# Optimization experiments

Hardware: AMD Instinct MI355X
Metric: run time of the kernel (lower is better)

## Reference

```python
import jax, jax.numpy as jnp
import numpy as np

B, S, HID = 2, 2048, 2048
H, KV, D = 16, 8, 128
EPS = 1e-6
MROPE = [21, 21, 22]  # half_dim=64 -> [64//3, 64//3, 64-2*(64//3)]
SCALE = D ** -0.5


def setup_inputs() -> dict:
    key = jax.random.key(0)
    ks = jax.random.split(key, 8)
    hidden_states = jax.random.normal(ks[0], (B, S, HID), jnp.float32)
    # 3D mrope cos/sin: one position grid per modality axis (use same arange positions)
    inv_freq = 1.0 / (10000.0 ** (jnp.arange(0, D, 2, dtype=jnp.float32) / D))  # [64]
    pos = jnp.arange(S, dtype=jnp.float32)
    freqs = pos[:, None] * inv_freq[None, :]                  # [S, 64]
    emb = jnp.concatenate([freqs, freqs], axis=-1)            # [S, 128]
    cos = jnp.broadcast_to(jnp.cos(emb)[None, None], (3, B, S, D)).astype(jnp.float32)
    sin = jnp.broadcast_to(jnp.sin(emb)[None, None], (3, B, S, D)).astype(jnp.float32)
    q_w = jax.random.normal(ks[1], (H * D, HID), jnp.float32) * 0.02
    k_w = jax.random.normal(ks[2], (KV * D, HID), jnp.float32) * 0.02
    v_w = jax.random.normal(ks[3], (KV * D, HID), jnp.float32) * 0.02
    o_w = jax.random.normal(ks[4], (HID, H * D), jnp.float32) * 0.02
    q_norm_w = jnp.ones((D,), jnp.float32)
    k_norm_w = jnp.ones((D,), jnp.float32)
    return dict(hidden_states=hidden_states, cos=cos, sin=sin, q_w=q_w, k_w=k_w,
                v_w=v_w, o_w=o_w, q_norm_w=q_norm_w, k_norm_w=k_norm_w)


def _rmsnorm(x, w):
    var = jnp.mean(jnp.square(x.astype(jnp.float32)), axis=-1, keepdims=True)
    return (x * jax.lax.rsqrt(var + EPS)).astype(x.dtype) * w


def _rotate_half(x):
    x1, x2 = jnp.split(x, 2, axis=-1)
    return jnp.concatenate([-x2, x1], axis=-1)


def _mrope_mix(t):
    # t: [3, B, S, D]; split last dim into mrope_section*2 chunks, pick chunk i from axis-0 index i%3
    sections = MROPE * 2
    idx = np.cumsum(sections)[:-1]
    chunks = jnp.split(t, idx, axis=-1)
    mixed = jnp.concatenate([c[i % 3] for i, c in enumerate(chunks)], axis=-1)  # [B, S, D]
    return mixed[:, None, :, :]  # unsqueeze head dim -> [B, 1, S, D]


def reference(hidden_states, cos, sin, q_w, k_w, v_w, o_w, q_norm_w, k_norm_w):
    # QKV projections -> [B, n_heads, S, D]
    q = (hidden_states @ q_w.T).reshape(B, S, H, D)
    k = (hidden_states @ k_w.T).reshape(B, S, KV, D)
    v = (hidden_states @ v_w.T).reshape(B, S, KV, D)
    q = _rmsnorm(q, q_norm_w).transpose(0, 2, 1, 3)   # [B, H, S, D]
    k = _rmsnorm(k, k_norm_w).transpose(0, 2, 1, 3)   # [B, KV, S, D]
    v = v.transpose(0, 2, 1, 3)                       # [B, KV, S, D]
    # 3D multimodal RoPE
    c = _mrope_mix(cos)
    s = _mrope_mix(sin)
    q = q * c + _rotate_half(q) * s
    k = k * c + _rotate_half(k) * s
    # GQA: repeat kv heads
    groups = H // KV
    k = jnp.repeat(k, groups, axis=1)  # [B, H, S, D]
    v = jnp.repeat(v, groups, axis=1)
    # causal SDPA (eager)
    scores = jnp.einsum('bhqd,bhkd->bhqk', q, k) * SCALE
    causal = jnp.tril(jnp.ones((S, S), bool))
    scores = jnp.where(causal[None, None], scores, jnp.finfo(scores.dtype).min)
    probs = jax.nn.softmax(scores, axis=-1)
    attn = jnp.einsum('bhqk,bhkd->bhqd', probs, v)     # [B, H, S, D]
    attn = attn.transpose(0, 2, 1, 3).reshape(B, S, H * D)
    return attn @ o_w.T
```

## Files before the change

kernel.cpp:

```cpp
#include <hip/hip_runtime.h>
#include <hip/hip_bf16.h>

typedef __attribute__((ext_vector_type(8))) short short8;
typedef __attribute__((ext_vector_type(4))) short short4v;
typedef __attribute__((ext_vector_type(4))) float f32x4;

#define B_ 2
#define S_ 2048
#define HID_ 2048
#define H_ 16
#define KV_ 8
#define D_ 128
#define SCALE_ 0.08838834764831845f

__device__ inline short f2bf(float f) {
    union { __hip_bfloat16 h; short s; } u;
    u.h = __float2bfloat16(f);
    return u.s;
}
__device__ inline float bf2f(short s) {
    union { short s; __hip_bfloat16 h; } u;
    u.s = s;
    return __bfloat162float(u.h);
}

__device__ inline void gld16(const short* g, short* l) {
    __builtin_amdgcn_global_load_lds(
        (const __attribute__((address_space(1))) unsigned int*)g,
        (__attribute__((address_space(3))) unsigned int*)l, 16, 0, 0);
}

__device__ inline int mrope_axis(int d) {
    int m = d & 63;
    return m < 21 ? 0 : (m < 42 ? 1 : 2);
}
__global__ __launch_bounds__(256) void prep(const float* __restrict__ hid,
                                            const float* __restrict__ qw_,
                                            const float* __restrict__ kw_,
                                            const float* __restrict__ vw_,
                                            const float* __restrict__ ow_,
                                            const float* __restrict__ cosp,
                                            const float* __restrict__ sinp,
                                            short* __restrict__ Hb,
                                            short* __restrict__ Wqkv,
                                            short* __restrict__ Owb,
                                            float* __restrict__ cm,
                                            float* __restrict__ sm) {
    int bid = blockIdx.x;
    if (bid < 20480) {
        const float* src; short* dst; int base;
        if (bid < 8192)       { src = hid; dst = Hb;              base = bid; }
        else if (bid < 12288) { src = qw_; dst = Wqkv;            base = bid - 8192; }
        else if (bid < 14336) { src = kw_; dst = Wqkv + 4194304;  base = bid - 12288; }
        else if (bid < 16384) { src = vw_; dst = Wqkv + 6291456;  base = bid - 14336; }
        else                  { src = ow_; dst = Owb;             base = bid - 16384; }
        int i = base * 1024 + threadIdx.x * 4;
        float4 v = *(const float4*)(&src[i]);
        short4v o;
        o.x = f2bf(v.x); o.y = f2bf(v.y); o.z = f2bf(v.z); o.w = f2bf(v.w);
        *(short4v*)(&dst[i]) = o;
    } else {
        const size_t AX = (size_t)B_ * S_ * D_;
        int i0 = (bid - 20480) * 1024 + threadIdx.x * 4;
#pragma unroll
        for (int k = 0; k < 4; ++k) {
            int idx = i0 + k;
            int d = idx & (D_ - 1);
            size_t src = (size_t)mrope_axis(d) * AX + idx;
            cm[idx] = cosp[src];
            sm[idx] = sinp[src];
        }
    }
}

__global__ __launch_bounds__(256) void gemm_bt(const short* __restrict__ A,
                                               const short* __restrict__ B,
                                               float* __restrict__ C,
                                               int M, int N, int K) {
    __shared__ __align__(16) short As[128 * 64];
    __shared__ __align__(16) short Bs[128 * 64];
    int tid = threadIdx.x;
    int wave = tid >> 6, lane = tid & 63;
    int m16 = lane & 15, quad = lane >> 4;
    int wr = wave >> 1, wc = wave & 1;
    int m0 = blockIdx.y * 128, n0 = blockIdx.x * 128;
    int srow = lane >> 3;
    int scol = ((lane & 7) ^ srow) << 3;
    f32x4 acc[4][4] = {};
    for (int k0 = 0; k0 < K; k0 += 64) {
#pragma unroll
        for (int i = 0; i < 4; ++i) {
            gld16(&A[(size_t)(m0 + wave * 32 + i * 8 + srow) * K + k0 + scol],
                  &As[(wave * 32 + i * 8) * 64]);
            gld16(&B[(size_t)(n0 + wave * 32 + i * 8 + srow) * K + k0 + scol],
                  &Bs[(wave * 32 + i * 8) * 64]);
        }
        __syncthreads();
        short8 a[4][2], b[4][2];
#pragma unroll
        for (int i = 0; i < 4; ++i)
#pragma unroll
            for (int kk = 0; kk < 2; ++kk) {
                int gsw = (((kk << 2) + quad) ^ (m16 & 7)) << 3;
                a[i][kk] = *(const short8*)(&As[(wr * 64 + i * 16 + m16) * 64 + gsw]);
                b[i][kk] = *(const short8*)(&Bs[(wc * 64 + i * 16 + m16) * 64 + gsw]);
            }
#pragma unroll
        for (int kk = 0; kk < 2; ++kk)
#pragma unroll
            for (int i = 0; i < 4; ++i)
#pragma unroll
                for (int j = 0; j < 4; ++j)
                    acc[i][j] = __builtin_amdgcn_mfma_f32_16x16x32_bf16(a[i][kk], b[j][kk],
                                                                        acc[i][j], 0, 0, 0);
        __syncthreads();
    }
#pragma unroll
    for (int i = 0; i < 4; ++i) {
        int row = m0 + wr * 64 + i * 16 + quad * 4;
#pragma unroll
        for (int j = 0; j < 4; ++j) {
            int col = n0 + wc * 64 + j * 16 + m16;
#pragma unroll
            for (int r = 0; r < 4; ++r)
                C[(size_t)(row + r) * N + col] = acc[i][j][r];
        }
    }
}


#define VM4 asm volatile("s_waitcnt vmcnt(4)" ::: "memory")
#define VM2 asm volatile("s_waitcnt vmcnt(2)" ::: "memory")
#define VM0 asm volatile("s_waitcnt vmcnt(0)" ::: "memory")

#define LDA(dst, QI)                                                               \
    _Pragma("unroll") for (int ii = 0; ii < 4; ++ii)                               \
        _Pragma("unroll") for (int kk = 0; kk < 2; ++kk)                           \
            dst[ii][kk] = *(const short8*)&lds[RA +                                \
                (wr * 128 + ((QI) * 4 + ii) * 16 + m16) * 64 +                     \
                ((((kk << 2) + quad) ^ (m16 & 7)) << 3)]

#define LDB(dst, QJ)                                                               \
    _Pragma("unroll") for (int jj = 0; jj < 2; ++jj)                               \
        _Pragma("unroll") for (int kk = 0; kk < 2; ++kk)                           \
            dst[jj][kk] = *(const short8*)&lds[RB +                                \
                ((QJ) * 128 + wc * 32 + jj * 16 + m16) * 64 +                      \
                ((((kk << 2) + quad) ^ (m16 & 7)) << 3)]

#define MM(ua, ub, QI, QJ)                                                         \
    _Pragma("unroll") for (int kk = 0; kk < 2; ++kk)                               \
        _Pragma("unroll") for (int ii = 0; ii < 4; ++ii)                           \
            _Pragma("unroll") for (int jj = 0; jj < 2; ++jj)                       \
                acc[(QI) * 4 + ii][(QJ) * 2 + jj] =                                \
                    __builtin_amdgcn_mfma_f32_16x16x32_bf16(                       \
                        ua[ii][kk], ub[jj][kk],                                    \
                        acc[(QI) * 4 + ii][(QJ) * 2 + jj], 0, 0, 0)

#define STGA(q) do {                                                               \
    int r_ = (wave << 3) + (lane >> 3);                                            \
    int g_ = (lane & 7) ^ (r_ & 7);                                                \
    gld16(&Am[(size_t)(m0 + (q) * 64 + r_) * 2048 + kc + (g_ << 3)],               \
          &lds[PA + (q) * 4096 + (wave << 9)]);                                    \
} while (0)
#define STGB(h, c) do {                                                            \
    int s_ = (wave << 3) + (lane >> 3);                                            \
    int sl_ = (h) * 128 + (c) * 64 + s_;                                           \
    int rr_ = ((sl_ >> 5) & 3) * 64 + (h) * 32 + (sl_ & 31);                       \
    int g_ = (lane & 7) ^ (sl_ & 7);                                               \
    gld16(&Bm[(size_t)(n0 + rr_) * 2048 + kc + (g_ << 3)],                         \
          &lds[PB + ((h) * 128 + (c) * 64) * 64 + (wave << 9)]);                   \
} while (0)

#define PH(LOADS, STG, MFMAS, WAITOP) do {                                         \
    LOADS;                                                                         \
    STG;                                                                           \
    __builtin_amdgcn_sched_barrier(0);                                             \
    __builtin_amdgcn_s_barrier();                                                  \
    asm volatile("s_waitcnt lgkmcnt(0)" ::: "memory");                             \
    __builtin_amdgcn_sched_barrier(0);                                             \
    __builtin_amdgcn_s_setprio(1);                                                 \
    MFMAS;                                                                         \
    __builtin_amdgcn_s_setprio(0);                                                 \
    WAITOP;                                                                        \
    __builtin_amdgcn_sched_barrier(0);                                             \
    __builtin_amdgcn_s_barrier();                                                  \
} while (0)

__global__ __launch_bounds__(512) void gemm_qkv(const short* __restrict__ Am,
                                                const short* __restrict__ Bm,
                                                short* __restrict__ Cq,
                                                short* __restrict__ Vb) {
    __shared__ __align__(16) char smem[131072];
    short* lds = (short*)smem;
    int tid = threadIdx.x;
    int wave = tid >> 6, lane = tid & 63;
    int m16 = lane & 15, quad = lane >> 4;
    int wr = wave >> 2, wc = wave & 3;
    int orig = blockIdx.y * 16 + blockIdx.x;
    int swz = (orig & 7) * 32 + (orig >> 3);
    int bx = swz & 15, by = swz >> 4;
    int m0 = by * 256, n0 = bx * 256;
    int x = bx;
    f32x4 acc[8][4] = {};

    {
        const int kc = 0, PA = 0, PB = 16384;
        STGA(0); STGA(1); STGA(2); STGA(3);
        STGB(0, 0); STGB(0, 1); STGB(1, 0); STGB(1, 1);
        VM0;
        __builtin_amdgcn_sched_barrier(0);
        __builtin_amdgcn_s_barrier();
    }

    short8 af[4][2], bfX[2][2], bfY[2][2];
    for (int t = 0; t < 31; ++t) {
        const int RA = (t & 1) << 15, RB = RA + 16384;
        const int PA = RA ^ 32768, PB = PA + 16384;
        const int kc = (t + 1) << 6;
        PH({ LDA(af, 0); LDB(bfX, 0); }, { STGA(0); STGA(2); },       MM(af, bfX, 0, 0), VM4);
        PH({ LDB(bfY, 1); },             { STGB(0, 0); STGB(0, 1); }, MM(af, bfY, 0, 1), VM4);
        PH({ LDA(af, 1); },              { STGB(1, 0); STGB(1, 1); }, MM(af, bfY, 1, 1), VM4);
        PH({ ; },                        { STGA(1); STGA(3); },       MM(af, bfX, 1, 0), VM4);
    }
    {
        const int RA = 32768, RB = RA + 16384;
        PH({ LDA(af, 0); LDB(bfX, 0); }, { ; }, MM(af, bfX, 0, 0), VM2);
        PH({ LDB(bfY, 1); },             { ; }, MM(af, bfY, 0, 1), VM0);
        PH({ LDA(af, 1); },              { ; }, MM(af, bfY, 1, 1), );
        PH({ ; },                        { ; }, MM(af, bfX, 1, 0), );
    }

    int bb = m0 >> 11, s0 = m0 & (S_ - 1);
    if (x >= 12) {
        short* T = (short*)smem;
        int kv0 = (x - 12) << 1;
        for (int hs = 0; hs < 2; ++hs) {
            __syncthreads();
            if (wr == hs) {
#pragma unroll
                for (int i = 0; i < 8; ++i)
#pragma unroll
                    for (int j = 0; j < 4; ++j) {
                        short4v v4;
#pragma unroll
                        for (int r = 0; r < 4; ++r) v4[r] = f2bf(acc[i][j][r]);
                        *(short4v*)&T[(wc * 64 + j * 16 + m16) * 136 + i * 16 + quad * 4] = v4;
                    }
            }
            __syncthreads();
#pragma unroll
            for (int it = 0; it < 8; ++it) {
                int e = (it * 512 + tid) * 8;
                int col = e >> 7, ro = e & 127;
                int kvh = col >> 7, d = col & 127;
                *(short8*)&Vb[(((size_t)(bb * KV_ + kv0 + kvh)) * D_ + d) * S_ +
                              s0 + hs * 128 + ro] =
                    *(const short8*)&T[col * 136 + ro];
            }
        }
    } else {
#pragma unroll
        for (int i = 0; i < 8; ++i) {
            int row = m0 + wr * 128 + i * 16 + quad * 4;
#pragma unroll
            for (int j = 0; j < 4; ++j) {
                int col = n0 + wc * 64 + j * 16 + m16;
#pragma unroll
                for (int r = 0; r < 4; ++r)
                    Cq[(size_t)(row + r) * 3072 + col] = f2bf(acc[i][j][r]);
            }
        }
    }
}

#undef PH
#undef LDA
#undef LDB
#undef MM
#undef STGA
#undef STGB
#undef VM4
#undef VM2
#undef VM0

#define TP 136
__global__ __launch_bounds__(256) void qkv_post(const short* __restrict__ Cq,
                                                const float* __restrict__ qnw,
                                                const float* __restrict__ knw,
                                                const float* __restrict__ cm,
                                                const float* __restrict__ sm,
                                                short* __restrict__ Qb,
                                                short* __restrict__ Kb) {
    __shared__ __align__(16) short T[128 * TP];
    __shared__ float sq[128];
    __shared__ float rsA[128];
    int tid = threadIdx.x;
    int hk = blockIdx.x;
    int m0 = blockIdx.y * 128;
    int b = m0 >> 11, s0 = m0 & (S_ - 1);
#pragma unroll
    for (int it = 0; it < 8; ++it) {
        int idx = it * 256 + tid;
        int row = idx >> 4, g = idx & 15;
        short8 v = *(const short8*)&Cq[(size_t)(m0 + row) * 3072 + hk * 128 + g * 8];
        *(short8*)&T[row * TP + g * 8] = v;
        float s = 0.f;
#pragma unroll
        for (int k = 0; k < 8; ++k) { float f = bf2f(v[k]); s += f * f; }
#pragma unroll
        for (int msk = 8; msk >= 1; msk >>= 1) s += __shfl_xor(s, msk, 64);
        if ((tid & 15) == 0) sq[row] = s;
    }
    __syncthreads();
    if (tid < 128) rsA[tid] = rsqrtf(sq[tid] * (1.0f / 128.0f) + 1e-6f);
    __syncthreads();
    const float* nw = (hk < 16) ? qnw : knw;
    short* outp = (hk < 16) ? (Qb + ((size_t)(b * H_ + hk)) * S_ * D_)
                            : (Kb + ((size_t)(b * KV_ + hk - 16)) * S_ * D_);
    size_t cmb = ((size_t)(b * S_ + s0)) * D_;
#pragma unroll
    for (int it = 0; it < 8; ++it) {
        int e = (it * 256 + tid) * 8;
        int row = e >> 7, colc = e & 127;
        int pc = colc ^ 64;
        float rs = rsA[row];
        float sg = (colc < 64) ? -1.f : 1.f;
        short8 nv = *(const short8*)&T[row * TP + colc];
        short8 pv = *(const short8*)&T[row * TP + pc];
        float4 cA = *(const float4*)&cm[cmb + (size_t)row * D_ + colc];
        float4 cB = *(const float4*)&cm[cmb + (size_t)row * D_ + colc + 4];
        float4 sA = *(const float4*)&sm[cmb + (size_t)row * D_ + colc];
        float4 sB = *(const float4*)&sm[cmb + (size_t)row * D_ + colc + 4];
        float4 wA = *(const float4*)&nw[colc];
        float4 wB = *(const float4*)&nw[colc + 4];
        float4 wpA = *(const float4*)&nw[pc];
        float4 wpB = *(const float4*)&nw[pc + 4];
        float cs[8] = {cA.x, cA.y, cA.z, cA.w, cB.x, cB.y, cB.z, cB.w};
        float sn[8] = {sA.x, sA.y, sA.z, sA.w, sB.x, sB.y, sB.z, sB.w};
        float wv[8] = {wA.x, wA.y, wA.z, wA.w, wB.x, wB.y, wB.z, wB.w};
        float wp[8] = {wpA.x, wpA.y, wpA.z, wpA.w, wpB.x, wpB.y, wpB.z, wpB.w};
        short8 o;
#pragma unroll
        for (int k = 0; k < 8; ++k) {
            float xv = bf2f(nv[k]) * rs * wv[k];
            float pvv = bf2f(pv[k]) * rs * wp[k];
            o[k] = f2bf(xv * cs[k] + sg * pvv * sn[k]);
        }
        *(short8*)&outp[(size_t)(s0 + row) * D_ + colc] = o;
    }
}

#define VPAD 72
__global__ __launch_bounds__(256) void attn_fa(const short* __restrict__ Qb,
                                               const short* __restrict__ Kb,
                                               const short* __restrict__ Vb,
                                               short* __restrict__ Ab) {
    __shared__ __align__(16) short Ks[2][64 * 128];
    __shared__ __align__(16) short Vs[2][128 * 64];
    __shared__ __align__(16) short Ps[4][16 * VPAD];
    int tid = threadIdx.x;
    int wave = tid >> 6, lane = tid & 63;
    int m16 = lane & 15, quad = lane >> 4;
    int bh = blockIdx.x;
    int h = bh & 15, b = bh >> 4;
    int qt = 31 - blockIdx.y;
    int kv = h >> 1;
    const short* Qp = Qb + (size_t)(b * H_ + h) * S_ * D_;
    const short* Kp = Kb + (size_t)(b * KV_ + kv) * S_ * D_;
    const short* Vp = Vb + (size_t)(b * KV_ + kv) * D_ * S_;
    int q_base = qt * 64 + wave * 16;
    int qrow = q_base + m16;
    short8 qf[4];
#pragma unroll
    for (int c = 0; c < 4; ++c)
        qf[c] = *(const short8*)(&Qp[(size_t)(q_base + m16) * D_ + c * 32 + quad * 8]);
    f32x4 o_acc[8] = {};
    float m_r = -1e30f, l_r = 0.f;
    int nchunks = qt + 1;

#pragma unroll
    for (int j = 0; j < 4; ++j) {
        int idx = wave * 4 + j;
        int r = idx * 4 + (lane >> 4);
        int g = (lane & 15) ^ (r & 7);
        gld16(&Kp[(size_t)r * D_ + g * 8], &Ks[0][idx * 512]);
    }
#pragma unroll
    for (int j = 0; j < 4; ++j) {
        int idx = wave * 4 + j;
        int r = idx * 8 + (lane >> 3);
        int g = (lane & 7) ^ (r & 7);
        gld16(&Vp[(size_t)r * S_ + g * 8], &Vs[0][idx * 512]);
    }
    __syncthreads();

    for (int kc = 0; kc < nchunks; ++kc) {
        int k0 = kc * 64;
        int cur = kc & 1;
        if (kc + 1 < nchunks) {
            int nk0 = k0 + 64, nb = cur ^ 1;
#pragma unroll
            for (int j = 0; j < 4; ++j) {
                int idx = wave * 4 + j;
                int r = idx * 4 + (lane >> 4);
                int g = (lane & 15) ^ (r & 7);
                gld16(&Kp[(size_t)(nk0 + r) * D_ + g * 8], &Ks[nb][idx * 512]);
            }
#pragma unroll
            for (int j = 0; j < 4; ++j) {
                int idx = wave * 4 + j;
                int r = idx * 8 + (lane >> 3);
                int g = (lane & 7) ^ (r & 7);
                gld16(&Vp[(size_t)r * S_ + nk0 + g * 8], &Vs[nb][idx * 512]);
            }
        }
        float sv[4][4];
        __builtin_amdgcn_s_setprio(1);
#pragma unroll
        for (int nt = 0; nt < 4; ++nt) {
            f32x4 facc = {};
#pragma unroll
            for (int c = 0; c < 4; ++c) {
                short8 kfr = *(const short8*)(&Ks[cur][(nt * 16 + m16) * 128 +
                                                      ((((c << 2) + quad) ^ (m16 & 7)) << 3)]);
                facc = __builtin_amdgcn_mfma_f32_16x16x32_bf16(kfr, qf[c], facc, 0, 0, 0);
            }
            if (kc == qt) {
#pragma unroll
                for (int r = 0; r < 4; ++r) {
                    int key = k0 + nt * 16 + quad * 4 + r;
                    sv[nt][r] = (key <= qrow) ? facc[r] * SCALE_ : -1e30f;
                }
            } else {
#pragma unroll
                for (int r = 0; r < 4; ++r) sv[nt][r] = facc[r] * SCALE_;
            }
        }
        __builtin_amdgcn_s_setprio(0);
        float mx = -1e30f;
#pragma unroll
        for (int nt = 0; nt < 4; ++nt)
#pragma unroll
            for (int r = 0; r < 4; ++r) mx = fmaxf(mx, sv[nt][r]);
        mx = fmaxf(mx, __shfl_xor(mx, 16, 64));
        mx = fmaxf(mx, __shfl_xor(mx, 32, 64));
        float m_new = fmaxf(m_r, mx);
        float alpha = __expf(m_r - m_new);
        float p[4][4], sum = 0.f;
#pragma unroll
        for (int nt = 0; nt < 4; ++nt)
#pragma unroll
            for (int r = 0; r < 4; ++r) { p[nt][r] = __expf(sv[nt][r] - m_new); sum += p[nt][r]; }
        sum += __shfl_xor(sum, 16, 64);
        sum += __shfl_xor(sum, 32, 64);
        l_r = l_r * alpha + sum;
        m_r = m_new;
#pragma unroll
        for (int nt = 0; nt < 4; ++nt) {
            short4v pk;
#pragma unroll
            for (int r = 0; r < 4; ++r) pk[r] = f2bf(p[nt][r]);
            *(short4v*)&Ps[wave][m16 * VPAD + nt * 16 + quad * 4] = pk;
        }
#pragma unroll
        for (int j = 0; j < 8; ++j) {
            f32x4 t = o_acc[j];
#pragma unroll
            for (int r = 0; r < 4; ++r) t[r] *= alpha;
            o_acc[j] = t;
        }
        __builtin_amdgcn_s_setprio(1);
#pragma unroll
        for (int kk = 0; kk < 2; ++kk) {
            short8 pf = *(const short8*)(&Ps[wave][m16 * VPAD + kk * 32 + quad * 8]);
#pragma unroll
            for (int j = 0; j < 8; ++j) {
                short8 vfr = *(const short8*)(&Vs[cur][(j * 16 + m16) * 64 +
                                                       ((((kk << 2) + quad) ^ (m16 & 7)) << 3)]);
                o_acc[j] = __builtin_amdgcn_mfma_f32_16x16x32_bf16(vfr, pf, o_acc[j], 0, 0, 0);
            }
        }
        __builtin_amdgcn_s_setprio(0);
        __syncthreads();
    }
    float inv_l = 1.0f / l_r;
    size_t base = ((size_t)(b * S_ + qrow)) * (H_ * D_) + h * D_;
#pragma unroll
    for (int j = 0; j < 8; ++j) {
        short4v ov;
#pragma unroll
        for (int r = 0; r < 4; ++r) ov[r] = f2bf(o_acc[j][r] * inv_l);
        *(short4v*)&Ab[base + j * 16 + quad * 4] = ov;
    }
}

extern "C" void kernel_launch(void* const* d_in, const int* in_sizes, int n_in,
                              void* d_out, int out_size, void* d_ws, size_t ws_size,
                              hipStream_t stream) {
    const float* hid  = (const float*)d_in[0];
    const float* cosp = (const float*)d_in[1];
    const float* sinp = (const float*)d_in[2];
    const float* q_w  = (const float*)d_in[3];
    const float* k_w  = (const float*)d_in[4];
    const float* v_w  = (const float*)d_in[5];
    const float* o_w  = (const float*)d_in[6];
    const float* qnw  = (const float*)d_in[7];
    const float* knw  = (const float*)d_in[8];

    char* w = (char*)d_ws;
    short* Hb    = (short*)w;  w += (size_t)4096 * 2048 * 2;
    short* Wqkv  = (short*)w;  w += (size_t)4096 * 2048 * 2;
    short* Owb   = (short*)w;  w += (size_t)2048 * 2048 * 2;
    short* Qb    = (short*)w;  w += (size_t)B_ * H_ * S_ * D_ * 2;
    short* Kb    = (short*)w;  w += (size_t)B_ * KV_ * S_ * D_ * 2;
    short* Vb    = (short*)w;  w += (size_t)B_ * KV_ * D_ * S_ * 2;
    short* Ab    = (short*)w;  w += (size_t)4096 * 2048 * 2;
    float* cos_m = (float*)w;  w += (size_t)B_ * S_ * D_ * 4;
    float* sin_m = (float*)w;  w += (size_t)B_ * S_ * D_ * 4;
    short* Cq    = (short*)w;  w += (size_t)4096 * 3072 * 2;

    prep<<<20992, 256, 0, stream>>>(hid, q_w, k_w, v_w, o_w, cosp, sinp,
                                    Hb, Wqkv, Owb, cos_m, sin_m);

    gemm_qkv<<<dim3(16, 16), 512, 0, stream>>>(Hb, Wqkv, Cq, Vb);

    qkv_post<<<dim3(24, 32), 256, 0, stream>>>(Cq, qnw, knw, cos_m, sin_m, Qb, Kb);

    attn_fa<<<dim3(32, 32), 256, 0, stream>>>(Qb, Kb, Vb, Ab);

    gemm_bt<<<dim3(16, 32), 256, 0, stream>>>(Ab, Owb, (float*)d_out, 4096, 2048, 2048);
}
```

Baseline: 329.6 us.

## Process two 64-row query tiles per attention block to reuse K/V tiles

Each attention block now handles 128 query rows (two 16-row subtiles per wave) so every K/V tile loaded into LDS feeds twice the MFMA work, halving the grid. Softmax switches to exp2 with a folded scale via raw v_exp_f32, and the rescale of the accumulator is skipped unless the running max grows past a threshold (lazy rescaling). The cost is doubled accumulator registers, which may lower occupancy, plus fewer blocks for load balance.

```diff
diff --git a/kernel.cpp b/kernel.cpp
--- a/kernel.cpp
+++ b/kernel.cpp
@@ -12,6 +12,8 @@
 #define KV_ 8
 #define D_ 128
 #define SCALE_ 0.08838834764831845f
+#define SC2_ 0.12751743f
+#define THRRAW_ 62.7f
 
 __device__ inline short f2bf(float f) {
     union { __hip_bfloat16 h; short s; } u;
@@ -22,6 +24,9 @@
     union { short s; __hip_bfloat16 h; } u;
     u.s = s;
     return __bfloat162float(u.h);
+}
+__device__ inline float ex2(float x) {
+    float r; asm("v_exp_f32 %0, %1" : "=v"(r) : "v"(x)); return r;
 }
 
 __device__ inline void gld16(const short* g, short* l) {
@@ -363,20 +368,22 @@
     int m16 = lane & 15, quad = lane >> 4;
     int bh = blockIdx.x;
     int h = bh & 15, b = bh >> 4;
-    int qt = 31 - blockIdx.y;
+    int qt = 15 - blockIdx.y;
     int kv = h >> 1;
     const short* Qp = Qb + (size_t)(b * H_ + h) * S_ * D_;
     const short* Kp = Kb + (size_t)(b * KV_ + kv) * S_ * D_;
     const short* Vp = Vb + (size_t)(b * KV_ + kv) * D_ * S_;
-    int q_base = qt * 64 + wave * 16;
-    int qrow = q_base + m16;
-    short8 qf[4];
-#pragma unroll
-    for (int c = 0; c < 4; ++c)
-        qf[c] = *(const short8*)(&Qp[(size_t)(q_base + m16) * D_ + c * 32 + quad * 8]);
-    f32x4 o_acc[8] = {};
-    float m_r = -1e30f, l_r = 0.f;
-    int nchunks = qt + 1;
+    int qrow0 = qt * 128 + wave * 16 + m16;
+    int qrow1 = qrow0 + 64;
+    short8 qf0[4], qf1[4];
+#pragma unroll
+    for (int c = 0; c < 4; ++c) {
+        qf0[c] = *(const short8*)(&Qp[(size_t)qrow0 * D_ + c * 32 + quad * 8]);
+        qf1[c] = *(const short8*)(&Qp[(size_t)qrow1 * D_ + c * 32 + quad * 8]);
+    }
+    f32x4 o0[8] = {}, o1[8] = {};
+    float m0r = -1e30f, l0r = 0.f, m1r = -1e30f, l1r = 0.f;
+    int nchunks = 2 * qt + 2;
 
 #pragma unroll
     for (int j = 0; j < 4; ++j) {
@@ -394,6 +401,52 @@
     }
     __syncthreads();
 
+#define SMAX(sv, mr, lr, oA, p) do {                                              \
+    float mx = -1e30f;                                                            \
+    _Pragma("unroll") for (int nt = 0; nt < 4; ++nt)                              \
+        _Pragma("unroll") for (int r = 0; r < 4; ++r) mx = fmaxf(mx, sv[nt][r]);  \
+    mx = fmaxf(mx, __shfl_xor(mx, 16, 64));                                       \
+    mx = fmaxf(mx, __shfl_xor(mx, 32, 64));                                       \
+    if (!__all(mx - mr <= THRRAW_)) {                                             \
+        float mn = fmaxf(mr, mx);                                                 \
+        float al = ex2((mr - mn) * SC2_);                                         \
+        _Pragma("unroll") for (int j = 0; j < 8; ++j) {                           \
+            f32x4 t = oA[j];                                                      \
+            _Pragma("unroll") for (int r = 0; r < 4; ++r) t[r] *= al;             \
+            oA[j] = t;                                                            \
+        }                                                                         \
+        lr *= al; mr = mn;                                                        \
+    }                                                                             \
+    float ms = mr * SC2_;                                                         \
+    float sum = 0.f;                                                              \
+    _Pragma("unroll") for (int nt = 0; nt < 4; ++nt)                              \
+        _Pragma("unroll") for (int r = 0; r < 4; ++r) {                           \
+            p[nt][r] = ex2(__builtin_fmaf(sv[nt][r], SC2_, -ms));                 \
+            sum += p[nt][r];                                                      \
+        }                                                                         \
+    sum += __shfl_xor(sum, 16, 64);                                               \
+    sum += __shfl_xor(sum, 32, 64);                                               \
+    lr += sum;                                                                    \
+} while (0)
+
+#define PVSTEP(p, oA) do {                                                        \
+    _Pragma("unroll") for (int nt = 0; nt < 4; ++nt) {                            \
+        short4v pk;                                                               \
+        _Pragma("unroll") for (int r = 0; r < 4; ++r) pk[r] = f2bf(p[nt][r]);     \
+        *(short4v*)&Ps[wave][m16 * VPAD + nt * 16 + quad * 4] = pk;               \
+    }                                                                             \
+    __builtin_amdgcn_s_setprio(1);                                                \
+    _Pragma("unroll") for (int kk = 0; kk < 2; ++kk) {                            \
+        short8 pf = *(const short8*)(&Ps[wave][m16 * VPAD + kk * 32 + quad * 8]); \
+        _Pragma("unroll") for (int j = 0; j < 8; ++j) {                           \
+            short8 vfr = *(const short8*)(&Vs[cur][(j * 16 + m16) * 64 +          \
+                                 ((((kk << 2) + quad) ^ (m16 & 7)) << 3)]);       \
+            oA[j] = __builtin_amdgcn_mfma_f32_16x16x32_bf16(vfr, pf, oA[j], 0, 0, 0); \
+        }                                                                         \
+    }                                                                             \
+    __builtin_amdgcn_s_setprio(0);                                                \
+} while (0)
+
     for (int kc = 0; kc < nchunks; ++kc) {
         int k0 = kc * 64;
         int cur = kc & 1;
@@ -414,83 +467,79 @@
                 gld16(&Vp[(size_t)r * S_ + nk0 + g * 8], &Vs[nb][idx * 512]);
             }
         }
-        float sv[4][4];
+        bool do0 = (kc < nchunks - 1);
+        bool dg0 = (kc == nchunks - 2);
+        bool dg1 = (kc == nchunks - 1);
+        float sv0[4][4], sv1[4][4];
         __builtin_amdgcn_s_setprio(1);
 #pragma unroll
         for (int nt = 0; nt < 4; ++nt) {
-            f32x4 facc = {};
-#pragma unroll
-            for (int c = 0; c < 4; ++c) {
-                short8 kfr = *(const short8*)(&Ks[cur][(nt * 16 + m16) * 128 +
-                                                      ((((c << 2) + quad) ^ (m16 & 7)) << 3)]);
-                facc = __builtin_amdgcn_mfma_f32_16x16x32_bf16(kfr, qf[c], facc, 0, 0, 0);
-            }
-            if (kc == qt) {
+            short8 kfr[4];
+#pragma unroll
+            for (int c = 0; c < 4; ++c)
+                kfr[c] = *(const short8*)(&Ks[cur][(nt * 16 + m16) * 128 +
+                                      ((((c << 2) + quad) ^ (m16 & 7)) << 3)]);
+            f32x4 f1a = {};
+#pragma unroll
+            for (int c = 0; c < 4; ++c)
+                f1a = __builtin_amdgcn_mfma_f32_16x16x32_bf16(kfr[c], qf1[c], f1a, 0, 0, 0);
+            if (do0) {
+                f32x4 f0a = {};
+#pragma unroll
+                for (int c = 0; c < 4; ++c)
+                    f0a = __builtin_amdgcn_mfma_f32_16x16x32_bf16(kfr[c], qf0[c], f0a, 0, 0, 0);
+#pragma unroll
+                for (int r = 0; r < 4; ++r) sv0[nt][r] = f0a[r];
+            }
+#pragma unroll
+            for (int r = 0; r < 4; ++r) sv1[nt][r] = f1a[r];
+        }
+        __builtin_amdgcn_s_setprio(0);
+        if (dg0) {
+#pragma unroll
+            for (int nt = 0; nt < 4; ++nt)
 #pragma unroll
                 for (int r = 0; r < 4; ++r) {
                     int key = k0 + nt * 16 + quad * 4 + r;
-                    sv[nt][r] = (key <= qrow) ? facc[r] * SCALE_ : -1e30f;
+                    if (key > qrow0) sv0[nt][r] = -1e30f;
                 }
-            } else {
-#pragma unroll
-                for (int r = 0; r < 4; ++r) sv[nt][r] = facc[r] * SCALE_;
-            }
-        }
-        __builtin_amdgcn_s_setprio(0);
-        float mx = -1e30f;
-#pragma unroll
-        for (int nt = 0; nt < 4; ++nt)
-#pragma unroll
-            for (int r = 0; r < 4; ++r) mx = fmaxf(mx, sv[nt][r]);
-        mx = fmaxf(mx, __shfl_xor(mx, 16, 64));
-        mx = fmaxf(mx, __shfl_xor(mx, 32, 64));
-        float m_new = fmaxf(m_r, mx);
-        float alpha = __expf(m_r - m_new);
-        float p[4][4], sum = 0.f;
-#pragma unroll
-        for (int nt = 0; nt < 4; ++nt)
-#pragma unroll
-            for (int r = 0; r < 4; ++r) { p[nt][r] = __expf(sv[nt][r] - m_new); sum += p[nt][r]; }
-        sum += __shfl_xor(sum, 16, 64);
-        sum += __shfl_xor(sum, 32, 64);
-        l_r = l_r * alpha + sum;
-        m_r = m_new;
-#pragma unroll
-        for (int nt = 0; nt < 4; ++nt) {
-            short4v pk;
-#pragma unroll
-            for (int r = 0; r < 4; ++r) pk[r] = f2bf(p[nt][r]);
-            *(short4v*)&Ps[wave][m16 * VPAD + nt * 16 + quad * 4] = pk;
-        }
-#pragma unroll
-        for (int j = 0; j < 8; ++j) {
-            f32x4 t = o_acc[j];
-#pragma unroll
-            for (int r = 0; r < 4; ++r) t[r] *= alpha;
-            o_acc[j] = t;
-        }
-        __builtin_amdgcn_s_setprio(1);
-#pragma unroll
-        for (int kk = 0; kk < 2; ++kk) {
-            short8 pf = *(const short8*)(&Ps[wave][m16 * VPAD + kk * 32 + quad * 8]);
-#pragma unroll
-            for (int j = 0; j < 8; ++j) {
-                short8 vfr = *(const short8*)(&Vs[cur][(j * 16 + m16) * 64 +
-                                                       ((((kk << 2) + quad) ^ (m16 & 7)) << 3)]);
-                o_acc[j] = __builtin_amdgcn_mfma_f32_16x16x32_bf16(vfr, pf, o_acc[j], 0, 0, 0);
-            }
-        }
-        __builtin_amdgcn_s_setprio(0);
+        }
+        if (dg1) {
+#pragma unroll
+            for (int nt = 0; nt < 4; ++nt)
+#pragma unroll
+                for (int r = 0; r < 4; ++r) {
+                    int key = k0 + nt * 16 + quad * 4 + r;
+                    if (key > qrow1) sv1[nt][r] = -1e30f;
+                }
+        }
+        if (do0) {
+            float p0[4][4];
+            SMAX(sv0, m0r, l0r, o0, p0);
+            PVSTEP(p0, o0);
+        }
+        {
+            float p1[4][4];
+            SMAX(sv1, m1r, l1r, o1, p1);
+            PVSTEP(p1, o1);
+        }
         __syncthreads();
     }
-    float inv_l = 1.0f / l_r;
-    size_t base = ((size_t)(b * S_ + qrow)) * (H_ * D_) + h * D_;
+#undef SMAX
+#undef PVSTEP
+    float il0 = 1.0f / l0r, il1 = 1.0f / l1r;
+    size_t base0 = ((size_t)(b * S_ + qrow0)) * (H_ * D_) + h * D_;
+    size_t base1 = ((size_t)(b * S_ + qrow1)) * (H_ * D_) + h * D_;
 #pragma unroll
     for (int j = 0; j < 8; ++j) {
-        short4v ov;
-#pragma unroll
-        for (int r = 0; r < 4; ++r) ov[r] = f2bf(o_acc[j][r] * inv_l);
-        *(short4v*)&Ab[base + j * 16 + quad * 4] = ov;
+        short4v ov0, ov1;
+#pragma unroll
+        for (int r = 0; r < 4; ++r) {
+            ov0[r] = f2bf(o0[j][r] * il0);
+            ov1[r] = f2bf(o1[j][r] * il1);
+        }
+        *(short4v*)&Ab[base0 + j * 16 + quad * 4] = ov0;
+        *(short4v*)&Ab[base1 + j * 16 + quad * 4] = ov1;
     }
 }
 
@@ -526,7 +575,7 @@
 
     qkv_post<<<dim3(24, 32), 256, 0, stream>>>(Cq, qnw, knw, cos_m, sin_m, Qb, Kb);
 
-    attn_fa<<<dim3(32, 32), 256, 0, stream>>>(Qb, Kb, Vb, Ab);
+    attn_fa<<<dim3(32, 16), 256, 0, stream>>>(Qb, Kb, Vb, Ab);
 
     gemm_bt<<<dim3(16, 32), 256, 0, stream>>>(Ab, Owb, (float*)d_out, 4096, 2048, 2048);
 }
```

Result: slower. 354.0 us (+7.4%).
